# Optimization experiments

Measured on AMD Instinct MI355X. Metric: run time of the kernel, lower is better.

The kernel has to match this reference:

```python
import jax, jax.numpy as jnp
import numpy as np

# Fixed architecture constants (hardcoded in PPGEncoder)
B_DEF, C_IN, L_SEQ = 64, 4, 256
H, N_STATE, N_BLOCKS = 4, 4, 2  # d_model, SSM state size, n_blocks


def _layernorm(v, scale, bias, eps=1e-5):
    mu = v.mean(-1, keepdims=True)
    var = v.var(-1, keepdims=True)
    return (v - mu) / jnp.sqrt(var + eps) * scale + bias


def _avgpool1d(v, out_size):
    # AdaptiveAvgPool1d where out_size divides L evenly -> block mean
    b, c, l = v.shape
    return v.reshape(b, c, out_size, l // out_size).mean(-1)


def setup_inputs() -> dict:
    key = jax.random.key(0)
    ks = iter(jax.random.split(key, 40))
    nrm = lambda shape, s=1.0: jax.random.normal(next(ks), shape, jnp.float32) * s
    inp = {
        "x": nrm((B_DEF, C_IN, L_SEQ)),
        # S4 encoder / decoder linears
        "enc_W": nrm((C_IN, H), 0.5), "enc_b": jnp.zeros((H,), jnp.float32),
        # per-block S4D params, stacked over blocks
        "ln_s": jnp.ones((N_BLOCKS, H), jnp.float32), "ln_b": jnp.zeros((N_BLOCKS, H), jnp.float32),
        "log_dt": jax.random.uniform(next(ks), (N_BLOCKS, H), jnp.float32,
                                      minval=float(np.log(1e-3)), maxval=float(np.log(1e-1))),
        "A_re": nrm((N_BLOCKS, H, N_STATE), 0.5),
        "A_im": jnp.tile(jnp.pi * jnp.arange(N_STATE, dtype=jnp.float32), (N_BLOCKS, H, 1)),
        "C_re": nrm((N_BLOCKS, H, N_STATE), 0.5), "C_im": nrm((N_BLOCKS, H, N_STATE), 0.5),
        "D": nrm((N_BLOCKS, H), 1.0),
        "out_W": nrm((N_BLOCKS, H, H), 0.5), "out_b": jnp.zeros((N_BLOCKS, H), jnp.float32),
        "dec_W": nrm((H, H), 0.5), "dec_b": jnp.zeros((H,), jnp.float32),
        # projection MLP: Linear(1856,1024) LN ReLU Linear(1024,4096) LN ReLU Unflatten(512,8) Linear(8,4096)
        "W1": nrm((1856, 1024), 0.02), "b1": jnp.zeros((1024,), jnp.float32),
        "g1": jnp.ones((1024,), jnp.float32), "be1": jnp.zeros((1024,), jnp.float32),
        "W2": nrm((1024, 4096), 0.02), "b2": jnp.zeros((4096,), jnp.float32),
        "g2": jnp.ones((4096,), jnp.float32), "be2": jnp.zeros((4096,), jnp.float32),
        "W3": nrm((8, 4096), 0.3), "b3": jnp.zeros((4096,), jnp.float32),
    }
    return inp


def _s4_model(x, enc_W, enc_b, ln_s, ln_b, log_dt, A_re, A_im, C_re, C_im, D,
              out_W, out_b, dec_W, dec_b):
    # x: [B, C_IN, L]; S4Model consumes [B, L, d_input]
    L = x.shape[-1]
    u = jnp.einsum('bcl,ch->blh', x, enc_W) + enc_b  # [B,L,H]
    t = jnp.arange(L, dtype=jnp.float32)
    for i in range(ln_s.shape[0]):
        z = _layernorm(u, ln_s[i], ln_b[i])          # prenorm
        zc = jnp.swapaxes(z, 1, 2)                   # [B,H,L]
        dt = jnp.exp(log_dt[i])                      # [H]
        A = -jnp.exp(A_re[i]) + 1j * A_im[i]         # stable diag SSM [H,N]
        dtA = A * dt[:, None]
        Bd = (jnp.exp(dtA) - 1.0) / A                # ZOH input discretization
        C = C_re[i] + 1j * C_im[i]
        vand = jnp.exp(dtA[:, :, None] * t)          # [H,N,L] Vandermonde
        K = 2.0 * jnp.real(jnp.einsum('hn,hnl->hl', C * Bd, vand))  # [H,L]
        # causal FFT convolution + skip D
        Uf = jnp.fft.rfft(zc, n=2 * L)
        Kf = jnp.fft.rfft(K, n=2 * L)
        y = jnp.fft.irfft(Uf * Kf, n=2 * L)[..., :L] + D[i][:, None] * zc
        y = jax.nn.gelu(y)
        y = jnp.einsum('bhl,hk->blk', y, out_W[i]) + out_b[i]
        u = u + y                                    # residual
    return u @ dec_W + dec_b                         # [B,L,H]


def reference(x, enc_W, enc_b, ln_s, ln_b, log_dt, A_re, A_im, C_re, C_im, D,
              out_W, out_b, dec_W, dec_b, W1, b1, g1, be1, W2, b2, g2, be2, W3, b3):
    b = x.shape[0]
    s4_out = _s4_model(x, enc_W, enc_b, ln_s, ln_b, log_dt, A_re, A_im,
                       C_re, C_im, D, out_W, out_b, dec_W, dec_b)  # [B,L,H]
    zc = jnp.swapaxes(s4_out, 1, 2)                  # [B,H,L]
    z16 = _avgpool1d(zc, 16)                         # [B,4,16]
    # FeaturePyramidPooling on raw x: sizes 64,128,256
    fpp = jnp.concatenate([_avgpool1d(x, 64), _avgpool1d(x, 128), _avgpool1d(x, 256)], axis=-1)
    combined = jnp.concatenate([z16.reshape(b, -1), fpp.reshape(b, -1)], axis=1)  # [B,1856]
    h = jax.nn.relu(_layernorm(combined @ W1 + b1, g1, be1))   # [B,1024] (dropout=eval identity)
    h = jax.nn.relu(_layernorm(h @ W2 + b2, g2, be2))          # [B,4096]
    h = h.reshape(b, 512, 8)
    return h @ W3 + b3                                         # [B,512,4096]
```

## Files before the change

### kernel.cpp

```cpp
#include <hip/hip_runtime.h>
#include <hip/hip_bf16.h>
#include <math.h>

#define BDEF 64
#define LSEQ 256
#define HD   4
#define NST  4
#define NBLK 2

typedef float nfloat4 __attribute__((ext_vector_type(4)));

__device__ inline void nt_store4(const float4 v, float* p) {
    nfloat4 nv = {v.x, v.y, v.z, v.w};
    __builtin_nontemporal_store(nv, (nfloat4*)p);
}

#define ACCROW(accv, av)                                        \
    accv.x += av.x*w0.x + av.y*w1.x + av.z*w2.x + av.w*w3.x;    \
    accv.y += av.x*w0.y + av.y*w1.y + av.z*w2.y + av.w*w3.y;    \
    accv.z += av.x*w0.z + av.y*w1.z + av.z*w2.z + av.w*w3.z;    \
    accv.w += av.x*w0.w + av.y*w1.w + av.z*w2.w + av.w*w3.w;

__global__ __launch_bounds__(256) void s4front(
    const float* __restrict__ x, const float* __restrict__ enc_W,
    const float* __restrict__ enc_b, const float* __restrict__ ln_s,
    const float* __restrict__ ln_b, const float* __restrict__ log_dt,
    const float* __restrict__ A_re, const float* __restrict__ A_im,
    const float* __restrict__ C_re, const float* __restrict__ C_im,
    const float* __restrict__ Dp, const float* __restrict__ out_W,
    const float* __restrict__ out_b, const float* __restrict__ dec_W,
    const float* __restrict__ dec_b, float* __restrict__ combined)
{
    const int b = blockIdx.x;
    const int l = threadIdx.x;
    __shared__ float Kl[NBLK][LSEQ][4];
    __shared__ float x_lds[4][256];
    __shared__ float z_lds[256][4];
    __shared__ float s4_lds[256][4];

    {
        const float t = (float)l;
        for (int i = 0; i < NBLK; ++i) {
            #pragma unroll
            for (int h = 0; h < HD; ++h) {
                float dt = expf(log_dt[i*HD + h]);
                float acc = 0.f;
                #pragma unroll
                for (int n = 0; n < NST; ++n) {
                    const int idx = (i*HD + h)*NST + n;
                    float ar = -expf(A_re[idx]);
                    float ai = A_im[idx];
                    float dr = ar*dt, di = ai*dt;
                    float er  = expf(dr);
                    float e1r = er*cosf(di) - 1.0f;
                    float e1i = er*sinf(di);
                    float inv = 1.0f/(ar*ar + ai*ai);
                    float bdr = (e1r*ar + e1i*ai)*inv;
                    float bdi = (e1i*ar - e1r*ai)*inv;
                    float cr = C_re[idx], ci = C_im[idx];
                    float cbr = cr*bdr - ci*bdi;
                    float cbi = cr*bdi + ci*bdr;
                    float em = expf(dr*t);
                    float vr = em*cosf(di*t);
                    float vi = em*sinf(di*t);
                    acc += cbr*vr - cbi*vi;
                }
                Kl[i][l][h] = 2.0f*acc;
            }
        }
    }

    #pragma unroll
    for (int c = 0; c < 4; ++c)
        x_lds[c][l] = x[(b*4 + c)*256 + l];

    float u[4];
    #pragma unroll
    for (int h = 0; h < 4; ++h) {
        float a = enc_b[h];
        #pragma unroll
        for (int c = 0; c < 4; ++c) a += x_lds[c][l]*enc_W[c*4 + h];
        u[h] = a;
    }
    __syncthreads();

    for (int i = 0; i < NBLK; ++i) {
        float mu = 0.25f*(u[0]+u[1]+u[2]+u[3]);
        float var = 0.f;
        #pragma unroll
        for (int h = 0; h < 4; ++h) { float d = u[h]-mu; var += d*d; }
        var *= 0.25f;
        float rs = rsqrtf(var + 1e-5f);
        float z[4];
        #pragma unroll
        for (int h = 0; h < 4; ++h)
            z[h] = (u[h]-mu)*rs*ln_s[i*4 + h] + ln_b[i*4 + h];
        *(float4*)&z_lds[l][0] = make_float4(z[0], z[1], z[2], z[3]);
        __syncthreads();

        float y0 = 0.f, y1 = 0.f, y2 = 0.f, y3 = 0.f;
        const int mlim = l | 63;
        #pragma unroll 4
        for (int m = 0; m <= mlim; ++m) {
            float4 kk = *(const float4*)&Kl[i][m][0];
            int p = (l - m) & 255;
            float4 zz = *(const float4*)&z_lds[p][0];
            if (m <= l) {
                y0 += kk.x*zz.x; y1 += kk.y*zz.y;
                y2 += kk.z*zz.z; y3 += kk.w*zz.w;
            }
        }
        float y[4] = {y0, y1, y2, y3};
        #pragma unroll
        for (int h = 0; h < 4; ++h) {
            float v = y[h] + Dp[i*4 + h]*z[h];
            float inner = 0.7978845608028654f*(v + 0.044715f*v*v*v);
            y[h] = 0.5f*v*(1.0f + tanhf(inner));
        }
        #pragma unroll
        for (int k = 0; k < 4; ++k) {
            float a = out_b[i*4 + k];
            #pragma unroll
            for (int h = 0; h < 4; ++h) a += y[h]*out_W[(i*4 + h)*4 + k];
            u[k] += a;
        }
        __syncthreads();
    }

    #pragma unroll
    for (int h = 0; h < 4; ++h) {
        float a = dec_b[h];
        #pragma unroll
        for (int k = 0; k < 4; ++k) a += u[k]*dec_W[k*4 + h];
        s4_lds[l][h] = a;
    }
    __syncthreads();

    float* cmb = combined + b*1856;
    if (l < 64) {
        int h = l >> 4, kk = l & 15;
        float a = 0.f;
        #pragma unroll
        for (int j = 0; j < 16; ++j) a += s4_lds[kk*16 + j][h];
        cmb[l] = a*(1.0f/16.0f);
    }
    for (int e = l; e < 1792; e += 256) {
        int c = e/448, jj = e%448;
        float v;
        if (jj < 64) {
            v = 0.25f*(x_lds[c][4*jj] + x_lds[c][4*jj+1] +
                       x_lds[c][4*jj+2] + x_lds[c][4*jj+3]);
        } else if (jj < 192) {
            int q = jj - 64;
            v = 0.5f*(x_lds[c][2*q] + x_lds[c][2*q+1]);
        } else {
            v = x_lds[c][jj - 192];
        }
        cmb[64 + e] = v;
    }
}

template<int NCOLS, int ASTRIDE, int KCH>
__global__ __launch_bounds__(256) void mlp_part(
    const float* __restrict__ A, const float* __restrict__ W,
    float* __restrict__ parts)
{
    constexpr int APAD = KCH + 4;
    __shared__ float At[64][APAD];
    __shared__ float Wl[KCH][64];
    const int ks = blockIdx.x, k0 = ks*KCH;
    const int j0 = blockIdx.y*64;
    const int t  = threadIdx.x;

    {
        constexpr int AF4 = 64*KCH/4;
        constexpr int RF4 = KCH/4;
        #pragma unroll
        for (int f = t; f < AF4; f += 256) {
            const int row = f / RF4, c4 = f % RF4;
            *(float4*)&At[row][c4*4] =
                *(const float4*)(A + (size_t)row*ASTRIDE + k0 + c4*4);
        }
        constexpr int WF4 = KCH*16;
        #pragma unroll
        for (int f = t; f < WF4; f += 256) {
            const int row = f >> 4, c4 = f & 15;
            *(float4*)&Wl[row][c4*4] =
                *(const float4*)(W + (size_t)(k0 + row)*NCOLS + j0 + c4*4);
        }
    }
    __syncthreads();

    const int ji = t & 15, br = (t >> 4)*4;
    float4 acc0={0,0,0,0}, acc1={0,0,0,0}, acc2={0,0,0,0}, acc3={0,0,0,0};
    #pragma unroll 4
    for (int k4 = 0; k4 < KCH; k4 += 4) {
        float4 w0 = *(float4*)&Wl[k4+0][ji*4];
        float4 w1 = *(float4*)&Wl[k4+1][ji*4];
        float4 w2 = *(float4*)&Wl[k4+2][ji*4];
        float4 w3 = *(float4*)&Wl[k4+3][ji*4];
        float4 a0 = *(float4*)&At[br+0][k4];
        float4 a1 = *(float4*)&At[br+1][k4];
        float4 a2 = *(float4*)&At[br+2][k4];
        float4 a3 = *(float4*)&At[br+3][k4];
        ACCROW(acc0, a0) ACCROW(acc1, a1) ACCROW(acc2, a2) ACCROW(acc3, a3)
    }
    float* pbase = parts + (size_t)(ks*64 + br)*NCOLS + j0 + ji*4;
    *(float4*)(pbase)           = acc0;
    *(float4*)(pbase + NCOLS)   = acc1;
    *(float4*)(pbase + 2*NCOLS) = acc2;
    *(float4*)(pbase + 3*NCOLS) = acc3;
}

template<int N>
__global__ __launch_bounds__(256) void reduce_ln_relu(
    const float* __restrict__ parts, const float* __restrict__ bias,
    const float* __restrict__ g, const float* __restrict__ be,
    float* __restrict__ out, int KS)
{
    constexpr int NV = N/1024;
    const int b = blockIdx.x, t = threadIdx.x;
    float4 acc[NV];
    #pragma unroll
    for (int v = 0; v < NV; ++v)
        acc[v] = *(const float4*)(bias + v*1024 + t*4);
    for (int ks = 0; ks < KS; ++ks) {
        const float* p = parts + (size_t)(ks*64 + b)*N;
        #pragma unroll
        for (int v = 0; v < NV; ++v) {
            float4 q = *(const float4*)(p + v*1024 + t*4);
            acc[v].x += q.x; acc[v].y += q.y; acc[v].z += q.z; acc[v].w += q.w;
        }
    }
    float s = 0.f, s2 = 0.f;
    #pragma unroll
    for (int v = 0; v < NV; ++v) {
        s  += acc[v].x + acc[v].y + acc[v].z + acc[v].w;
        s2 += acc[v].x*acc[v].x + acc[v].y*acc[v].y +
              acc[v].z*acc[v].z + acc[v].w*acc[v].w;
    }
    #pragma unroll
    for (int off = 32; off > 0; off >>= 1) {
        s  += __shfl_down(s,  off);
        s2 += __shfl_down(s2, off);
    }
    __shared__ float red[2][4];
    const int w = t >> 6;
    if ((t & 63) == 0) { red[0][w] = s; red[1][w] = s2; }
    __syncthreads();
    float ts  = red[0][0] + red[0][1] + red[0][2] + red[0][3];
    float ts2 = red[1][0] + red[1][1] + red[1][2] + red[1][3];
    const float inv_n = 1.0f/(float)N;
    float mu  = ts*inv_n;
    float var = ts2*inv_n - mu*mu;
    float rs  = rsqrtf(var + 1e-5f);
    #pragma unroll
    for (int v = 0; v < NV; ++v) {
        const int j = v*1024 + t*4;
        float4 gv  = *(const float4*)(g + j);
        float4 bev = *(const float4*)(be + j);
        float4 o;
        o.x = fmaxf((acc[v].x - mu)*rs*gv.x + bev.x, 0.f);
        o.y = fmaxf((acc[v].y - mu)*rs*gv.y + bev.y, 0.f);
        o.z = fmaxf((acc[v].z - mu)*rs*gv.z + bev.z, 0.f);
        o.w = fmaxf((acc[v].w - mu)*rs*gv.w + bev.w, 0.f);
        *(float4*)(out + (size_t)b*N + j) = o;
    }
}

#define ROWS_D 64
__global__ __launch_bounds__(256) void final_mm(
    const float* __restrict__ h2, const float* __restrict__ W3,
    const float* __restrict__ b3, float* __restrict__ out)
{
    const int rg = blockIdx.x;
    const int js = blockIdx.y;
    const int t  = threadIdx.x;
    const int bs0 = rg*ROWS_D;
    const int j = js*1024 + t*4;
    float4 w[8];
    #pragma unroll
    for (int k = 0; k < 8; ++k) w[k] = *(const float4*)(W3 + k*4096 + j);
    const float4 bv = *(const float4*)(b3 + j);
    const float* __restrict__ hrow = h2 + (size_t)bs0*8;
    float* __restrict__ obase = out + (size_t)bs0*4096 + j;
    #pragma unroll 4
    for (int r = 0; r < ROWS_D; ++r) {
        float4 acc = bv;
        #pragma unroll
        for (int k = 0; k < 8; ++k) {
            const float hv = hrow[r*8 + k];
            acc.x += hv*w[k].x; acc.y += hv*w[k].y;
            acc.z += hv*w[k].z; acc.w += hv*w[k].w;
        }
        nt_store4(acc, obase + (size_t)r*4096);
    }
}

extern "C" void kernel_launch(void* const* d_in, const int* in_sizes, int n_in,
                              void* d_out, int out_size, void* d_ws, size_t ws_size,
                              hipStream_t stream) {
    const float* x      = (const float*)d_in[0];
    const float* enc_W  = (const float*)d_in[1];
    const float* enc_b  = (const float*)d_in[2];
    const float* ln_s   = (const float*)d_in[3];
    const float* ln_b   = (const float*)d_in[4];
    const float* log_dt = (const float*)d_in[5];
    const float* A_re   = (const float*)d_in[6];
    const float* A_im   = (const float*)d_in[7];
    const float* C_re   = (const float*)d_in[8];
    const float* C_im   = (const float*)d_in[9];
    const float* Dp     = (const float*)d_in[10];
    const float* out_W  = (const float*)d_in[11];
    const float* out_b  = (const float*)d_in[12];
    const float* dec_W  = (const float*)d_in[13];
    const float* dec_b  = (const float*)d_in[14];
    const float* W1     = (const float*)d_in[15];
    const float* b1     = (const float*)d_in[16];
    const float* g1     = (const float*)d_in[17];
    const float* be1    = (const float*)d_in[18];
    const float* W2     = (const float*)d_in[19];
    const float* b2     = (const float*)d_in[20];
    const float* g2     = (const float*)d_in[21];
    const float* be2    = (const float*)d_in[22];
    const float* W3     = (const float*)d_in[23];
    const float* b3     = (const float*)d_in[24];
    float* out = (float*)d_out;

    float* ws = (float*)d_ws;
    float* combined = ws;
    float* parts1   = combined + 64*1856;
    float* h1       = parts1 + 29*64*1024;
    float* parts2   = h1 + 64*1024;
    float* h2       = parts2 + 8*64*4096;

    s4front<<<64, 256, 0, stream>>>(x, enc_W, enc_b, ln_s, ln_b, log_dt,
                                    A_re, A_im, C_re, C_im, Dp,
                                    out_W, out_b, dec_W, dec_b, combined);
    mlp_part<1024,1856,64><<<dim3(29,16), 256, 0, stream>>>(combined, W1, parts1);
    reduce_ln_relu<1024><<<64, 256, 0, stream>>>(parts1, b1, g1, be1, h1, 29);
    mlp_part<4096,1024,128><<<dim3(8,64), 256, 0, stream>>>(h1, W2, parts2);
    reduce_ln_relu<4096><<<64, 256, 0, stream>>>(parts2, b2, g2, be2, h2, 8);
    final_mm<<<dim3(512,4), 256, 0, stream>>>(h2, W3, b3, out);
}
```

Before: 189.5 us.

## Split S4 causal convolution across 4 thread groups and halve W2 K-chunk

The S4 front kernel now runs 1024 threads per batch. Four groups each handle a 64-wide slice of the causal convolution over m, and the partial sums are reduced through shared memory. The kernel coefficients for the two blocks are computed by separate thread groups. Separately, the second MLP GEMM uses a smaller K chunk with twice as many K splits, so more blocks run but the reduction reads twice as many partial buffers. The goal is more parallelism in the latency-bound front kernel and the GEMM, at the cost of extra syncs and more partial-sum traffic.

New measurement: 166.1 us, median of 2. 1.14x faster.

```diff
diff --git a/kernel.cpp b/kernel.cpp
--- a/kernel.cpp
+++ b/kernel.cpp
@@ -7,6 +7,7 @@
 #define HD   4
 #define NST  4
 #define NBLK 2
+#define SPLIT 4
 
 typedef float nfloat4 __attribute__((ext_vector_type(4)));
 
@@ -21,7 +22,7 @@
     accv.z += av.x*w0.z + av.y*w1.z + av.z*w2.z + av.w*w3.z;    \
     accv.w += av.x*w0.w + av.y*w1.w + av.z*w2.w + av.w*w3.w;
 
-__global__ __launch_bounds__(256) void s4front(
+__global__ __launch_bounds__(1024) void s4front(
     const float* __restrict__ x, const float* __restrict__ enc_W,
     const float* __restrict__ enc_b, const float* __restrict__ ln_s,
     const float* __restrict__ ln_b, const float* __restrict__ log_dt,
@@ -31,48 +32,53 @@
     const float* __restrict__ out_b, const float* __restrict__ dec_W,
     const float* __restrict__ dec_b, float* __restrict__ combined)
 {
-    const int b = blockIdx.x;
-    const int l = threadIdx.x;
+    const int b    = blockIdx.x;
+    const int t    = threadIdx.x;
+    const int l    = t & 255;
+    const int part = t >> 8;
     __shared__ float Kl[NBLK][LSEQ][4];
     __shared__ float x_lds[4][256];
     __shared__ float z_lds[256][4];
     __shared__ float s4_lds[256][4];
-
-    {
-        const float t = (float)l;
-        for (int i = 0; i < NBLK; ++i) {
+    __shared__ float yp[SPLIT][256][4];
+
+    if (t < 512) {
+        const int i = part;
+        const float tt = (float)l;
+        #pragma unroll
+        for (int h = 0; h < HD; ++h) {
+            float dt = expf(log_dt[i*HD + h]);
+            float acc = 0.f;
             #pragma unroll
-            for (int h = 0; h < HD; ++h) {
-                float dt = expf(log_dt[i*HD + h]);
-                float acc = 0.f;
-                #pragma unroll
-                for (int n = 0; n < NST; ++n) {
-                    const int idx = (i*HD + h)*NST + n;
-                    float ar = -expf(A_re[idx]);
-                    float ai = A_im[idx];
-                    float dr = ar*dt, di = ai*dt;
-                    float er  = expf(dr);
-                    float e1r = er*cosf(di) - 1.0f;
-                    float e1i = er*sinf(di);
-                    float inv = 1.0f/(ar*ar + ai*ai);
-                    float bdr = (e1r*ar + e1i*ai)*inv;
-                    float bdi = (e1i*ar - e1r*ai)*inv;
-                    float cr = C_re[idx], ci = C_im[idx];
-                    float cbr = cr*bdr - ci*bdi;
-                    float cbi = cr*bdi + ci*bdr;
-                    float em = expf(dr*t);
-                    float vr = em*cosf(di*t);
-                    float vi = em*sinf(di*t);
-                    acc += cbr*vr - cbi*vi;
-                }
-                Kl[i][l][h] = 2.0f*acc;
+            for (int n = 0; n < NST; ++n) {
+                const int idx = (i*HD + h)*NST + n;
+                float ar = -expf(A_re[idx]);
+                float ai = A_im[idx];
+                float dr = ar*dt, di = ai*dt;
+                float er  = expf(dr);
+                float e1r = er*cosf(di) - 1.0f;
+                float e1i = er*sinf(di);
+                float inv = 1.0f/(ar*ar + ai*ai);
+                float bdr = (e1r*ar + e1i*ai)*inv;
+                float bdi = (e1i*ar - e1r*ai)*inv;
+                float cr = C_re[idx], ci = C_im[idx];
+                float cbr = cr*bdr - ci*bdi;
+                float cbi = cr*bdi + ci*bdr;
+                float em = expf(dr*tt);
+                float vr = em*cosf(di*tt);
+                float vi = em*sinf(di*tt);
+                acc += cbr*vr - cbi*vi;
             }
-        }
-    }
-
-    #pragma unroll
-    for (int c = 0; c < 4; ++c)
-        x_lds[c][l] = x[(b*4 + c)*256 + l];
+            Kl[i][l][h] = 2.0f*acc;
+        }
+    }
+
+    if (part == 0) {
+        #pragma unroll
+        for (int c = 0; c < 4; ++c)
+            x_lds[c][l] = x[(b*4 + c)*256 + l];
+    }
+    __syncthreads();
 
     float u[4];
     #pragma unroll
@@ -82,7 +88,9 @@
         for (int c = 0; c < 4; ++c) a += x_lds[c][l]*enc_W[c*4 + h];
         u[h] = a;
     }
-    __syncthreads();
+
+    const int mlim = l | 63;
+    const int m0   = part*64;
 
     for (int i = 0; i < NBLK; ++i) {
         float mu = 0.25f*(u[0]+u[1]+u[2]+u[3]);
@@ -95,13 +103,14 @@
         #pragma unroll
         for (int h = 0; h < 4; ++h)
             z[h] = (u[h]-mu)*rs*ln_s[i*4 + h] + ln_b[i*4 + h];
-        *(float4*)&z_lds[l][0] = make_float4(z[0], z[1], z[2], z[3]);
+        if (part == 0)
+            *(float4*)&z_lds[l][0] = make_float4(z[0], z[1], z[2], z[3]);
         __syncthreads();
 
         float y0 = 0.f, y1 = 0.f, y2 = 0.f, y3 = 0.f;
-        const int mlim = l | 63;
+        const int mhi = min(m0 + 63, mlim);
         #pragma unroll 4
-        for (int m = 0; m <= mlim; ++m) {
+        for (int m = m0; m <= mhi; ++m) {
             float4 kk = *(const float4*)&Kl[i][m][0];
             int p = (l - m) & 255;
             float4 zz = *(const float4*)&z_lds[p][0];
@@ -110,7 +119,15 @@
                 y2 += kk.z*zz.z; y3 += kk.w*zz.w;
             }
         }
-        float y[4] = {y0, y1, y2, y3};
+        *(float4*)&yp[part][l][0] = make_float4(y0, y1, y2, y3);
+        __syncthreads();
+
+        float4 p0 = *(const float4*)&yp[0][l][0];
+        float4 p1 = *(const float4*)&yp[1][l][0];
+        float4 p2 = *(const float4*)&yp[2][l][0];
+        float4 p3 = *(const float4*)&yp[3][l][0];
+        float y[4] = { p0.x+p1.x+p2.x+p3.x, p0.y+p1.y+p2.y+p3.y,
+                       p0.z+p1.z+p2.z+p3.z, p0.w+p1.w+p2.w+p3.w };
         #pragma unroll
         for (int h = 0; h < 4; ++h) {
             float v = y[h] + Dp[i*4 + h]*z[h];
@@ -127,24 +144,26 @@
         __syncthreads();
     }
 
-    #pragma unroll
-    for (int h = 0; h < 4; ++h) {
-        float a = dec_b[h];
-        #pragma unroll
-        for (int k = 0; k < 4; ++k) a += u[k]*dec_W[k*4 + h];
-        s4_lds[l][h] = a;
+    if (part == 0) {
+        #pragma unroll
+        for (int h = 0; h < 4; ++h) {
+            float a = dec_b[h];
+            #pragma unroll
+            for (int k = 0; k < 4; ++k) a += u[k]*dec_W[k*4 + h];
+            s4_lds[l][h] = a;
+        }
     }
     __syncthreads();
 
     float* cmb = combined + b*1856;
-    if (l < 64) {
-        int h = l >> 4, kk = l & 15;
+    if (t < 64) {
+        int h = t >> 4, kk = t & 15;
         float a = 0.f;
         #pragma unroll
         for (int j = 0; j < 16; ++j) a += s4_lds[kk*16 + j][h];
-        cmb[l] = a*(1.0f/16.0f);
-    }
-    for (int e = l; e < 1792; e += 256) {
+        cmb[t] = a*(1.0f/16.0f);
+    }
+    for (int e = t; e < 1792; e += 1024) {
         int c = e/448, jj = e%448;
         float v;
         if (jj < 64) {
@@ -332,14 +351,14 @@
     float* parts1   = combined + 64*1856;
     float* h1       = parts1 + 29*64*1024;
     float* parts2   = h1 + 64*1024;
-    float* h2       = parts2 + 8*64*4096;
-
-    s4front<<<64, 256, 0, stream>>>(x, enc_W, enc_b, ln_s, ln_b, log_dt,
-                                    A_re, A_im, C_re, C_im, Dp,
-                                    out_W, out_b, dec_W, dec_b, combined);
+    float* h2       = parts2 + 16*64*4096;
+
+    s4front<<<64, 1024, 0, stream>>>(x, enc_W, enc_b, ln_s, ln_b, log_dt,
+                                     A_re, A_im, C_re, C_im, Dp,
+                                     out_W, out_b, dec_W, dec_b, combined);
     mlp_part<1024,1856,64><<<dim3(29,16), 256, 0, stream>>>(combined, W1, parts1);
     reduce_ln_relu<1024><<<64, 256, 0, stream>>>(parts1, b1, g1, be1, h1, 29);
-    mlp_part<4096,1024,128><<<dim3(8,64), 256, 0, stream>>>(h1, W2, parts2);
-    reduce_ln_relu<4096><<<64, 256, 0, stream>>>(parts2, b2, g2, be2, h2, 8);
+    mlp_part<4096,1024,64><<<dim3(16,64), 256, 0, stream>>>(h1, W2, parts2);
+    reduce_ln_relu<4096><<<64, 256, 0, stream>>>(parts2, b2, g2, be2, h2, 16);
     final_mm<<<dim3(512,4), 256, 0, stream>>>(h2, W3, b3, out);
 }
```
